# Kernel optimization log

Hardware: AMD Instinct MI355X
Metric: run time of the kernel (lower is better)

## Reference

```python
import jax, jax.numpy as jnp
import numpy as np

# Multi-scale feature pyramid (H, W) per level: strides 8/16/32/64 on a ~512px image
SHAPES = ((64, 64), (32, 32), (16, 16), (8, 8))
N_HEADS, N_LEVELS, N_POINTS = 8, 4, 4
D_MODEL = 256
HEAD_DIM = D_MODEL // N_HEADS


def setup_inputs() -> dict:
    key = jax.random.key(0)
    ks = jax.random.split(key, 11)
    B, C = 4, D_MODEL
    Lv = sum(h * w for h, w in SHAPES)  # 5440
    Lq = Lv  # encoder self-attention: queries are the flattened features
    scale = 0.02
    return {
        "query": jax.random.normal(ks[0], (B, Lq, C), jnp.float32),
        "reference_points": jax.random.uniform(ks[1], (B, Lq, N_LEVELS, 2), jnp.float32),
        "value": jax.random.normal(ks[2], (B, Lv, C), jnp.float32),
        "W_off": jax.random.normal(ks[3], (C, N_HEADS * N_LEVELS * N_POINTS * 2), jnp.float32) * scale,
        "b_off": jax.random.normal(ks[4], (N_HEADS * N_LEVELS * N_POINTS * 2,), jnp.float32) * 0.5,
        "W_attn": jax.random.normal(ks[5], (C, N_HEADS * N_LEVELS * N_POINTS), jnp.float32) * scale,
        "b_attn": jax.random.normal(ks[6], (N_HEADS * N_LEVELS * N_POINTS,), jnp.float32) * scale,
        "W_val": jax.random.normal(ks[7], (C, C), jnp.float32) * scale,
        "b_val": jax.random.normal(ks[8], (C,), jnp.float32) * scale,
        "W_out": jax.random.normal(ks[9], (C, C), jnp.float32) * scale,
        "b_out": jax.random.normal(ks[10], (C,), jnp.float32) * scale,
    }


def _bilinear_sample(val, grid, H, W):
    """Replicates F.grid_sample(mode='bilinear', padding_mode='zeros', align_corners=False).

    val:  [N, C, H, W]
    grid: [N, Lq, P, 2] in [-1, 1] (x, y order)
    returns: [N, C, Lq, P]
    """
    N, C = val.shape[0], val.shape[1]
    # unnormalize (align_corners=False)
    x = (grid[..., 0] + 1.0) * 0.5 * W - 0.5  # [N, Lq, P]
    y = (grid[..., 1] + 1.0) * 0.5 * H - 0.5
    x0 = jnp.floor(x)
    y0 = jnp.floor(y)
    wx = x - x0  # fractional parts
    wy = y - y0
    flat = val.reshape(N, C, H * W)

    def gather(xi, yi):
        valid = (xi >= 0) & (xi < W) & (yi >= 0) & (yi < H)
        xc = jnp.clip(xi, 0, W - 1).astype(jnp.int32)
        yc = jnp.clip(yi, 0, H - 1).astype(jnp.int32)
        idx = yc * W + xc  # [N, Lq, P]
        g = jax.vmap(lambda v, i: v[:, i])(flat, idx)  # [N, C, Lq, P]
        return g * valid[:, None, :, :].astype(val.dtype)

    out = (gather(x0, y0) * ((1 - wx) * (1 - wy))[:, None]
           + gather(x0 + 1, y0) * (wx * (1 - wy))[:, None]
           + gather(x0, y0 + 1) * ((1 - wx) * wy)[:, None]
           + gather(x0 + 1, y0 + 1) * (wx * wy)[:, None])
    return out


def _ms_deform_attn(query, reference_points, value, W_off, b_off, W_attn, b_attn,
                    W_val, b_val, W_out, b_out):
    B, Lq, C = query.shape
    val = value @ W_val + b_val  # [B, Lv, C]
    val = val.reshape(B, -1, N_HEADS, HEAD_DIM)

    offsets = (query @ W_off + b_off).reshape(B, Lq, N_HEADS, N_LEVELS, N_POINTS, 2)
    weights = jax.nn.softmax(
        (query @ W_attn + b_attn).reshape(B, Lq, N_HEADS, N_LEVELS * N_POINTS), axis=-1
    ).reshape(B, Lq, N_HEADS, N_LEVELS, N_POINTS)

    # offset normalizer: (W, H) per level
    offset_norm = jnp.array([[w, h] for h, w in SHAPES], jnp.float32)
    # ref_dim == 2 branch
    locs = reference_points[:, :, None, :, None, :] + offsets / offset_norm[None, None, None, :, None, :]
    grids = 2.0 * locs - 1.0  # [B, Lq, nh, nl, np, 2]

    acc = jnp.zeros((B * N_HEADS, HEAD_DIM, Lq), query.dtype)
    start = 0
    for lid, (H, W) in enumerate(SHAPES):
        # [B, HW, nh, hd] -> [B*nh, hd, H, W]
        v = val[:, start:start + H * W].transpose(0, 2, 3, 1).reshape(B * N_HEADS, HEAD_DIM, H, W)
        g = grids[:, :, :, lid].transpose(0, 2, 1, 3, 4).reshape(B * N_HEADS, Lq, N_POINTS, 2)
        s = _bilinear_sample(v, g, H, W)  # [B*nh, hd, Lq, np]
        w = weights[:, :, :, lid].transpose(0, 2, 1, 3).reshape(B * N_HEADS, 1, Lq, N_POINTS)
        acc = acc + (s * w).sum(-1)
        start += H * W

    out = acc.reshape(B, D_MODEL, Lq).transpose(0, 2, 1)  # [B, Lq, C]
    return out @ W_out + b_out


def reference(query, reference_points, value, W_off, b_off, W_attn, b_attn,
              W_val, b_val, W_out, b_out):
    return _ms_deform_attn(query, reference_points, value, W_off, b_off,
                           W_attn, b_attn, W_val, b_val, W_out, b_out)
```

## Files before the change

kernel.cpp:

```cpp
#include <hip/hip_runtime.h>


typedef __attribute__((ext_vector_type(8))) _Float16 half8;
typedef __attribute__((ext_vector_type(4))) float f32x4;

__device__ __forceinline__ half8 splat8(_Float16 v) {
    half8 r = {v, v, v, v, v, v, v, v};
    return r;
}

#define M_TOTAL 21760

__global__ __launch_bounds__(256) void prep_weights(
    const float* __restrict__ W_val, const float* __restrict__ W_off,
    const float* __restrict__ W_attn, const float* __restrict__ W_out,
    const float* __restrict__ b_off, const float* __restrict__ b_attn,
    _Float16* __restrict__ wt_val, _Float16* __restrict__ wt_qcat,
    _Float16* __restrict__ wt_out, float* __restrict__ bcat)
{
    const int r = blockIdx.x;
    const int k = threadIdx.x;
    if (r < 256) {
        wt_val[r * 256 + k] = (_Float16)W_val[k * 256 + r];
    } else if (r < 640) {
        const int n = r - 256;
        const float v = (n < 256) ? W_off[k * 256 + n] : W_attn[k * 128 + (n - 256)];
        wt_qcat[n * 256 + k] = (_Float16)v;
    } else if (r < 896) {
        const int n = r - 640;
        wt_out[n * 256 + k] = (_Float16)W_out[k * 256 + n];
    } else {
        bcat[k] = b_off[k];
        if (k < 128) bcat[256 + k] = b_attn[k];
    }
}

template <int NN, bool OUTF16>
__global__ __launch_bounds__(256) void gemm_mfma(
    const float* __restrict__ A, const _Float16* __restrict__ Bt,
    const float* __restrict__ bias, void* __restrict__ Cvoid)
{
    __shared__ _Float16 Ah[128 * 32];
    __shared__ _Float16 Bh[128 * 32];

    const int tid = threadIdx.x;
    const int bm = blockIdx.y * 128;
    const int bn = blockIdx.x * 128;
    const int wave = tid >> 6, lane = tid & 63;
    const int wm = (wave & 1) * 64, wn = (wave >> 1) * 64;
    const int ml = lane & 15, kq = (lane >> 4) * 8;

    const f32x4 zero4 = {0.f, 0.f, 0.f, 0.f};
    f32x4 acc[4][4];
#pragma unroll
    for (int i = 0; i < 4; ++i)
#pragma unroll
        for (int j = 0; j < 4; ++j) acc[i][j] = zero4;

    for (int kt = 0; kt < 8; ++kt) {
        const int k0 = kt * 32;
        half8 areg[2], breg[2];
#pragma unroll
        for (int u = 0; u < 2; ++u) {
            const int e = tid + u * 256;
            const int row = e >> 2, koff = (e & 3) * 8;
            const float* src = A + (size_t)(bm + row) * 256 + k0 + koff;
            const float4 lo = *(const float4*)src;
            const float4 hi = *(const float4*)(src + 4);
            areg[u] = half8{(_Float16)lo.x, (_Float16)lo.y, (_Float16)lo.z, (_Float16)lo.w,
                            (_Float16)hi.x, (_Float16)hi.y, (_Float16)hi.z, (_Float16)hi.w};
            breg[u] = *(const half8*)(Bt + (size_t)(bn + row) * 256 + k0 + koff);
        }
        __syncthreads();
#pragma unroll
        for (int u = 0; u < 2; ++u) {
            const int e = tid + u * 256;
            *(half8*)(Ah + e * 8) = areg[u];
            *(half8*)(Bh + e * 8) = breg[u];
        }
        __syncthreads();

        half8 af[4], bf[4];
#pragma unroll
        for (int i = 0; i < 4; ++i)
            af[i] = *(const half8*)(Ah + (wm + i * 16 + ml) * 32 + kq);
#pragma unroll
        for (int j = 0; j < 4; ++j)
            bf[j] = *(const half8*)(Bh + (wn + j * 16 + ml) * 32 + kq);
#pragma unroll
        for (int i = 0; i < 4; ++i)
#pragma unroll
            for (int j = 0; j < 4; ++j)
                acc[i][j] = __builtin_amdgcn_mfma_f32_16x16x32_f16(af[i], bf[j], acc[i][j], 0, 0, 0);
    }

    const int r0 = (lane >> 4) * 4;
#pragma unroll
    for (int j = 0; j < 4; ++j) {
        const int col = bn + wn + j * 16 + ml;
        const float bj = bias[col];
#pragma unroll
        for (int i = 0; i < 4; ++i) {
            const int row = bm + wm + i * 16 + r0;
#pragma unroll
            for (int r = 0; r < 4; ++r) {
                const float v = acc[i][j][r] + bj;
                if (OUTF16)
                    ((_Float16*)Cvoid)[(size_t)(row + r) * NN + col] = (_Float16)v;
                else
                    ((float*)Cvoid)[(size_t)(row + r) * NN + col] = v;
            }
        }
    }
}

__global__ __launch_bounds__(256) void sample_f16(
    const _Float16* __restrict__ valh,
    const float* __restrict__ refp,
    const _Float16* __restrict__ offh,
    float* __restrict__ acc_out)
{
    const int wave = threadIdx.x >> 6, lane = threadIdx.x & 63;
    const int q2 = lane >> 5, sl = lane & 31;
    const int bq = blockIdx.x * 8 + wave * 2 + q2;
    const int b = bq / 5440;
    const int h = sl >> 2;
    const int d8 = (sl & 3) * 8;

    const _Float16* off_row = offh + (size_t)bq * 384 + h * 32;
    const _Float16* att_row = offh + (size_t)bq * 384 + 256 + h * 16;
    const float* rp = refp + (size_t)bq * 8;

    float offv[32];
#pragma unroll
    for (int i = 0; i < 4; ++i) {
        const half8 t = *(const half8*)(off_row + i * 8);
#pragma unroll
        for (int j = 0; j < 8; ++j) offv[i * 8 + j] = (float)t[j];
    }
    float lg[16];
    {
        const half8 t0 = *(const half8*)(att_row);
        const half8 t1 = *(const half8*)(att_row + 8);
#pragma unroll
        for (int j = 0; j < 8; ++j) { lg[j] = (float)t0[j]; lg[8 + j] = (float)t1[j]; }
    }
    float mx = -1e30f;
#pragma unroll
    for (int i = 0; i < 16; ++i) mx = fmaxf(mx, lg[i]);
    float s = 0.f;
#pragma unroll
    for (int i = 0; i < 16; ++i) { lg[i] = __expf(lg[i] - mx); s += lg[i]; }
    const float inv = 1.f / s;

    const float4 rp01 = *(const float4*)rp;
    const float4 rp23 = *(const float4*)(rp + 4);
    const float rxs[4] = {rp01.x, rp01.z, rp23.x, rp23.z};
    const float rys[4] = {rp01.y, rp01.w, rp23.y, rp23.w};

    const int Ws_[4] = {64, 32, 16, 8};
    const int starts_[4] = {0, 4096, 5120, 5376};

    half8 acc = splat8((_Float16)0.f);
#pragma unroll
    for (int l = 0; l < 4; ++l) {
        const int W = Ws_[l];
        const float fW = (float)W;
        const _Float16* vbase = valh + ((size_t)(b * 5440 + starts_[l])) * 256 + h * 32 + d8;
        const float rx = rxs[l], ry = rys[l];
#pragma unroll
        for (int p = 0; p < 4; ++p) {
            const int pi = l * 4 + p;
            const float aw = lg[pi] * inv;
            const float x = fmaf(rx, fW, offv[pi * 2 + 0]) - 0.5f;
            const float y = fmaf(ry, fW, offv[pi * 2 + 1]) - 0.5f;
            const float x0f = floorf(x), y0f = floorf(y);
            const int x0 = (int)x0f, y0 = (int)y0f;
            const float wx = x - x0f, wy = y - y0f;
            const bool okx0 = ((unsigned)x0 < (unsigned)W);
            const bool okx1 = ((unsigned)(x0 + 1) < (unsigned)W);
            const bool oky0 = ((unsigned)y0 < (unsigned)W);
            const bool oky1 = ((unsigned)(y0 + 1) < (unsigned)W);
            const int xc0 = min(max(x0, 0), W - 1);
            const int xc1 = min(max(x0 + 1, 0), W - 1);
            const int yc0 = min(max(y0, 0), W - 1);
            const int yc1 = min(max(y0 + 1, 0), W - 1);
            const float w00 = (okx0 & oky0) ? (1.f - wx) * (1.f - wy) * aw : 0.f;
            const float w10 = (okx1 & oky0) ? wx * (1.f - wy) * aw : 0.f;
            const float w01 = (okx0 & oky1) ? (1.f - wx) * wy * aw : 0.f;
            const float w11 = (okx1 & oky1) ? wx * wy * aw : 0.f;

            const half8 c00 = *(const half8*)(vbase + (size_t)(yc0 * W + xc0) * 256);
            const half8 c10 = *(const half8*)(vbase + (size_t)(yc0 * W + xc1) * 256);
            const half8 c01 = *(const half8*)(vbase + (size_t)(yc1 * W + xc0) * 256);
            const half8 c11 = *(const half8*)(vbase + (size_t)(yc1 * W + xc1) * 256);

            acc += c00 * splat8((_Float16)w00);
            acc += c10 * splat8((_Float16)w10);
            acc += c01 * splat8((_Float16)w01);
            acc += c11 * splat8((_Float16)w11);
        }
    }

    float* dst = acc_out + (size_t)bq * 256 + h * 32 + d8;
    const float4 o0 = {(float)acc[0], (float)acc[1], (float)acc[2], (float)acc[3]};
    const float4 o1 = {(float)acc[4], (float)acc[5], (float)acc[6], (float)acc[7]};
    *(float4*)dst = o0;
    *(float4*)(dst + 4) = o1;
}

extern "C" void kernel_launch(void* const* d_in, const int* in_sizes, int n_in,
                              void* d_out, int out_size, void* d_ws, size_t ws_size,
                              hipStream_t stream) {
    const float* query  = (const float*)d_in[0];
    const float* refp   = (const float*)d_in[1];
    const float* value  = (const float*)d_in[2];
    const float* W_off  = (const float*)d_in[3];
    const float* b_off  = (const float*)d_in[4];
    const float* W_attn = (const float*)d_in[5];
    const float* b_attn = (const float*)d_in[6];
    const float* W_val  = (const float*)d_in[7];
    const float* b_val  = (const float*)d_in[8];
    const float* W_out  = (const float*)d_in[9];
    const float* b_out  = (const float*)d_in[10];
    float* out = (float*)d_out;

    const size_t M = M_TOTAL;

    _Float16* valh = (_Float16*)d_ws;
    _Float16* offh = valh + M * 256;
    float* acc32   = (float*)(offh + M * 384);
    _Float16* wtv  = (_Float16*)(acc32 + M * 256);
    _Float16* wtq  = wtv + 256 * 256;
    _Float16* wto  = wtq + 384 * 256;
    float* bcat    = (float*)(wto + 256 * 256);

    dim3 blk(256);
    prep_weights<<<dim3(897), blk, 0, stream>>>(W_val, W_off, W_attn, W_out,
                                                b_off, b_attn, wtv, wtq, wto, bcat);
    gemm_mfma<256, true ><<<dim3(2, 170), blk, 0, stream>>>(value, wtv, b_val, valh);
    gemm_mfma<384, true ><<<dim3(3, 170), blk, 0, stream>>>(query, wtq, bcat, offh);
    sample_f16<<<dim3(M / 8), blk, 0, stream>>>(valh, refp, offh, acc32);
    gemm_mfma<256, false><<<dim3(2, 170), blk, 0, stream>>>(acc32, wto, b_out, out);
}
```

Before: 186.2 us.

## Pre-convert inputs to fp16 and stage GEMM tiles via direct global-to-LDS loads

Adds a separate kernel that converts value and query to fp16, so the GEMMs can load fp16 A tiles straight into LDS with global_load_lds instead of going through registers with an in-loop conversion. The sampling kernel now writes its accumulator as fp16, halving that intermediate's traffic into the output GEMM. This adds one extra pass over the inputs and an extra launch, and rounds the sampling output to fp16 precision.

```diff
diff --git a/kernel.cpp b/kernel.cpp
--- a/kernel.cpp
+++ b/kernel.cpp
@@ -3,6 +3,13 @@
 
 typedef __attribute__((ext_vector_type(8))) _Float16 half8;
 typedef __attribute__((ext_vector_type(4))) float f32x4;
+
+typedef __attribute__((address_space(3))) unsigned int lds_uint;
+typedef const __attribute__((address_space(1))) unsigned int g_uint;
+
+__device__ __forceinline__ void load_lds16(const _Float16* g, _Float16* l) {
+    __builtin_amdgcn_global_load_lds((g_uint*)g, (lds_uint*)l, 16, 0, 0);
+}
 
 __device__ __forceinline__ half8 splat8(_Float16 v) {
     half8 r = {v, v, v, v, v, v, v, v};
@@ -35,10 +42,27 @@
     }
 }
 
-template <int NN, bool OUTF16>
-__global__ __launch_bounds__(256) void gemm_mfma(
-    const float* __restrict__ A, const _Float16* __restrict__ Bt,
-    const float* __restrict__ bias, void* __restrict__ Cvoid)
+__global__ __launch_bounds__(256) void cvt_f32_f16(
+    const float* __restrict__ value, const float* __restrict__ query,
+    _Float16* __restrict__ val16, _Float16* __restrict__ q16)
+{
+    const size_t per = (size_t)M_TOTAL * 256 / 8;
+    size_t idx = (size_t)blockIdx.x * 256 + threadIdx.x;
+    const float* src;
+    _Float16* dst;
+    if (idx < per) { src = value; dst = val16; }
+    else { src = query; dst = q16; idx -= per; }
+    const float4 lo = *(const float4*)(src + idx * 8);
+    const float4 hi = *(const float4*)(src + idx * 8 + 4);
+    half8 o = {(_Float16)lo.x, (_Float16)lo.y, (_Float16)lo.z, (_Float16)lo.w,
+               (_Float16)hi.x, (_Float16)hi.y, (_Float16)hi.z, (_Float16)hi.w};
+    *(half8*)(dst + idx * 8) = o;
+}
+
+__global__ __launch_bounds__(256) void gemm_f16(
+    const _Float16* __restrict__ A, const _Float16* __restrict__ Bt,
+    const float* __restrict__ bias, void* __restrict__ Cv,
+    int NN, int outf16)
 {
     __shared__ _Float16 Ah[128 * 32];
     __shared__ _Float16 Bh[128 * 32];
@@ -49,6 +73,8 @@
     const int wave = tid >> 6, lane = tid & 63;
     const int wm = (wave & 1) * 64, wn = (wave >> 1) * 64;
     const int ml = lane & 15, kq = (lane >> 4) * 8;
+    const int lr = lane >> 2;
+    const int lk = (lane & 3) * 8;
 
     const f32x4 zero4 = {0.f, 0.f, 0.f, 0.f};
     f32x4 acc[4][4];
@@ -59,24 +85,14 @@
 
     for (int kt = 0; kt < 8; ++kt) {
         const int k0 = kt * 32;
-        half8 areg[2], breg[2];
-#pragma unroll
-        for (int u = 0; u < 2; ++u) {
-            const int e = tid + u * 256;
-            const int row = e >> 2, koff = (e & 3) * 8;
-            const float* src = A + (size_t)(bm + row) * 256 + k0 + koff;
-            const float4 lo = *(const float4*)src;
-            const float4 hi = *(const float4*)(src + 4);
-            areg[u] = half8{(_Float16)lo.x, (_Float16)lo.y, (_Float16)lo.z, (_Float16)lo.w,
-                            (_Float16)hi.x, (_Float16)hi.y, (_Float16)hi.z, (_Float16)hi.w};
-            breg[u] = *(const half8*)(Bt + (size_t)(bn + row) * 256 + k0 + koff);
-        }
         __syncthreads();
 #pragma unroll
-        for (int u = 0; u < 2; ++u) {
-            const int e = tid + u * 256;
-            *(half8*)(Ah + e * 8) = areg[u];
-            *(half8*)(Bh + e * 8) = breg[u];
+        for (int t = 0; t < 2; ++t) {
+            const int row = wave * 32 + t * 16;
+            load_lds16(A + (size_t)(bm + row + lr) * 256 + k0 + lk,
+                       Ah + (size_t)row * 32);
+            load_lds16(Bt + (size_t)(bn + row + lr) * 256 + k0 + lk,
+                       Bh + (size_t)row * 32);
         }
         __syncthreads();
 
@@ -101,14 +117,14 @@
         const float bj = bias[col];
 #pragma unroll
         for (int i = 0; i < 4; ++i) {
-            const int row = bm + wm + i * 16 + r0;
+            const size_t rbase = (size_t)(bm + wm + i * 16 + r0) * NN + col;
 #pragma unroll
             for (int r = 0; r < 4; ++r) {
                 const float v = acc[i][j][r] + bj;
-                if (OUTF16)
-                    ((_Float16*)Cvoid)[(size_t)(row + r) * NN + col] = (_Float16)v;
+                if (outf16)
+                    ((_Float16*)Cv)[rbase + (size_t)r * NN] = (_Float16)v;
                 else
-                    ((float*)Cvoid)[(size_t)(row + r) * NN + col] = v;
+                    ((float*)Cv)[rbase + (size_t)r * NN] = v;
             }
         }
     }
@@ -118,7 +134,7 @@
     const _Float16* __restrict__ valh,
     const float* __restrict__ refp,
     const _Float16* __restrict__ offh,
-    float* __restrict__ acc_out)
+    _Float16* __restrict__ acc_out)
 {
     const int wave = threadIdx.x >> 6, lane = threadIdx.x & 63;
     const int q2 = lane >> 5, sl = lane & 31;
@@ -202,11 +218,7 @@
         }
     }
 
-    float* dst = acc_out + (size_t)bq * 256 + h * 32 + d8;
-    const float4 o0 = {(float)acc[0], (float)acc[1], (float)acc[2], (float)acc[3]};
-    const float4 o1 = {(float)acc[4], (float)acc[5], (float)acc[6], (float)acc[7]};
-    *(float4*)dst = o0;
-    *(float4*)(dst + 4) = o1;
+    *(half8*)(acc_out + (size_t)bq * 256 + h * 32 + d8) = acc;
 }
 
 extern "C" void kernel_launch(void* const* d_in, const int* in_sizes, int n_in,
@@ -227,19 +239,22 @@
 
     const size_t M = M_TOTAL;
 
-    _Float16* valh = (_Float16*)d_ws;
-    _Float16* offh = valh + M * 256;
-    float* acc32   = (float*)(offh + M * 384);
-    _Float16* wtv  = (_Float16*)(acc32 + M * 256);
-    _Float16* wtq  = wtv + 256 * 256;
-    _Float16* wto  = wtq + 384 * 256;
-    float* bcat    = (float*)(wto + 256 * 256);
+    _Float16* val16 = (_Float16*)d_ws;
+    _Float16* q16   = val16 + M * 256;
+    _Float16* valh  = q16 + M * 256;
+    _Float16* offh  = valh + M * 256;
+    _Float16* wtv   = offh + M * 384;
+    _Float16* wtq   = wtv + 256 * 256;
+    _Float16* wto   = wtq + 384 * 256;
+    float* bcat     = (float*)(wto + 256 * 256);
+    _Float16* acc16 = val16;
 
     dim3 blk(256);
     prep_weights<<<dim3(897), blk, 0, stream>>>(W_val, W_off, W_attn, W_out,
                                                 b_off, b_attn, wtv, wtq, wto, bcat);
-    gemm_mfma<256, true ><<<dim3(2, 170), blk, 0, stream>>>(value, wtv, b_val, valh);
-    gemm_mfma<384, true ><<<dim3(3, 170), blk, 0, stream>>>(query, wtq, bcat, offh);
-    sample_f16<<<dim3(M / 8), blk, 0, stream>>>(valh, refp, offh, acc32);
-    gemm_mfma<256, false><<<dim3(2, 170), blk, 0, stream>>>(acc32, wto, b_out, out);
-}
+    cvt_f32_f16<<<dim3(2 * M * 256 / 8 / 256), blk, 0, stream>>>(value, query, val16, q16);
+    gemm_f16<<<dim3(2, 170), blk, 0, stream>>>(val16, wtv, b_val, valh, 256, 1);
+    gemm_f16<<<dim3(3, 170), blk, 0, stream>>>(q16, wtq, bcat, offh, 384, 1);
+    sample_f16<<<dim3(M / 8), blk, 0, stream>>>(valh, refp, offh, acc16);
+    gemm_f16<<<dim3(2, 170), blk, 0, stream>>>(acc16, wto, b_out, out, 256, 0);
+}
```

Result: no change. 185.1 us (-0.6%).
